# Optimization experiments

Measured on AMD Instinct MI355X. Metric: run time of the kernel, lower is better.

## Reference

```python
import jax, jax.numpy as jnp
import numpy as np
from jax import lax

B, T, D, H, S = 256, 512, 256, 512, 8


def setup_inputs() -> dict:
    key = jax.random.key(0)
    ks = jax.random.split(key, 8)
    bound = 1.0 / np.sqrt(H)  # torch LSTMCell/Linear default init scale
    u = lambda k_, shp: jax.random.uniform(k_, shp, jnp.float32, -bound, bound)
    _input = jax.random.normal(ks[0], (B, T, D), jnp.float32)
    h0 = jax.random.normal(ks[1], (B, H), jnp.float32)
    c0 = jax.random.normal(ks[2], (B, H), jnp.float32)
    W_ih = u(ks[3], (4 * H, D))
    W_hh = u(ks[4], (4 * H, H))
    b_ih = u(ks[5], (4 * H,))
    b_hh = u(ks[6], (4 * H,))
    W_lin = u(ks[7], (D, H))
    b_lin = jnp.zeros((D,), jnp.float32)
    # random skip weights per module logic: w1~Bern; w2=1 if w1==0 else Bern; first S steps (1,0)
    rng = np.random.default_rng(0)
    w1 = rng.integers(0, 2, T)
    w2 = np.where(w1 == 0, 1, rng.integers(0, 2, T))
    w1[:S] = 1
    w2[:S] = 0
    return {
        "_input": _input, "h0": h0, "c0": c0,
        "W_ih": W_ih, "W_hh": W_hh, "b_ih": b_ih, "b_hh": b_hh,
        "W_lin": W_lin, "b_lin": b_lin,
        "w1": jnp.asarray(w1, jnp.int32), "w2": jnp.asarray(w2, jnp.int32),
        "time_steps": T, "skip_size": S,
    }


def _lstm_cell(x, h, c, W_ih, W_hh, b_ih, b_hh):
    gates = x @ W_ih.T + b_ih + h @ W_hh.T + b_hh  # [B, 4H]
    i, f, g, o = jnp.split(gates, 4, axis=-1)
    i, f, o = jax.nn.sigmoid(i), jax.nn.sigmoid(f), jax.nn.sigmoid(o)
    c_new = f * c + i * jnp.tanh(g)
    h_new = o * jnp.tanh(c_new)
    return h_new, c_new


def reference(_input, h0, c0, W_ih, W_hh, b_ih, b_hh, W_lin, b_lin, w1, w2, time_steps, skip_size):
    # decoder-mode RSCN: feed previous linear(h) as next input
    buf_h = jnp.repeat(h0[None], skip_size, axis=0)  # FIFO queue as ring buffer [S,B,H]
    buf_c = jnp.repeat(c0[None], skip_size, axis=0)

    def step(carry, xs):
        h_feed, h, c, bh, bc = carry
        w1t, w2t, t = xs
        h_new, c_new = _lstm_cell(h_feed, h, c, W_ih, W_hh, b_ih, b_hh)
        pos = t % skip_size
        skip_h, skip_c = bh[pos], bc[pos]  # queue.get() (oldest)
        bh = bh.at[pos].set(h_new)          # queue.put(new)
        bc = bc.at[pos].set(c_new)
        a = w1t.astype(h_new.dtype)
        b = w2t.astype(h_new.dtype)
        norm = 1.0 / (a + b)
        comb_h = (a * h_new + b * jnp.tanh(skip_h)) * norm
        comb_c = (a * c_new + b * jnp.tanh(skip_c)) * norm
        out = comb_h @ W_lin.T + b_lin  # [B, D]
        return (out, comb_h, comb_c, bh, bc), out

    xs = (w1[:time_steps], w2[:time_steps], jnp.arange(time_steps))
    carry0 = (_input[:, 0, :], h0, c0, buf_h, buf_c)
    (_, h_fin, c_fin, _, _), outs = lax.scan(step, carry0, xs)
    return outs.transpose(1, 0, 2), h_fin, c_fin  # [B,T,D], final (h, c)
```

## Files before the change

kernel.cpp:

```cpp
#include <hip/hip_runtime.h>
#include <math.h>

#define BB 256
#define TT 512
#define DD 256
#define HH 512
#define SS 8
#define G4H 2048
#define BH (BB*HH)
#define OUT_BASE ((size_t)BB*TT*DD)
#define NGRP 16
#define GR 16
#define XSLOT_U32 4096

typedef _Float16 f16;
typedef __attribute__((ext_vector_type(8)))  _Float16 f16x8;
typedef __attribute__((ext_vector_type(16))) float    f32x16;

__device__ __forceinline__ float sigm(float x) { return 1.f / (1.f + __expf(-x)); }
__device__ __forceinline__ float ftanh(float x) {
  x = fminf(15.f, fmaxf(-15.f, x));
  float e = __expf(-2.f * x);
  return (1.f - e) / (1.f + e);
}


__global__ __launch_bounds__(256) void prep_wbig16(
    const float* __restrict__ W_ih, const float* __restrict__ W_hh,
    const float* __restrict__ W_lin, f16* __restrict__ Wbig16)
{
  __shared__ float As[64][20];
  __shared__ float Bs[16][68];
  const int n0 = blockIdx.x * 64;
  const int j0 = blockIdx.y * 64;
  const int tid = threadIdx.x;
  const int tn = tid >> 4, tj = tid & 15;
  float acc[4][4] = {};
  for (int k0 = 0; k0 < DD; k0 += 16) {
    { int r = tid >> 2, c = (tid & 3) * 4;
      *(float4*)&As[r][c] = *(const float4*)&W_ih[(size_t)(n0 + r) * DD + k0 + c]; }
    { int r = tid >> 4, c = (tid & 15) * 4;
      *(float4*)&Bs[r][c] = *(const float4*)&W_lin[(size_t)(k0 + r) * HH + j0 + c]; }
    __syncthreads();
    #pragma unroll
    for (int k = 0; k < 16; ++k) {
      float a[4], bv[4];
      #pragma unroll
      for (int i = 0; i < 4; ++i) a[i] = As[tn*4+i][k];
      #pragma unroll
      for (int m = 0; m < 4; ++m) bv[m] = Bs[k][tj*4+m];
      #pragma unroll
      for (int i = 0; i < 4; ++i)
        #pragma unroll
        for (int m = 0; m < 4; ++m)
          acc[i][m] = fmaf(a[i], bv[m], acc[i][m]);
    }
    __syncthreads();
  }
  #pragma unroll
  for (int i = 0; i < 4; ++i) {
    int n = n0 + tn*4 + i;
    #pragma unroll
    for (int m = 0; m < 4; ++m) {
      int j = j0 + tj*4 + m;
      Wbig16[(size_t)n*HH + j] = (f16)(acc[i][m] + W_hh[(size_t)n*HH + j]);
    }
  }
}

__global__ void prep_bias(const float* __restrict__ b_ih, const float* __restrict__ b_hh,
                          const float* __restrict__ W_ih, const float* __restrict__ b_lin,
                          float* __restrict__ bias0, float* __restrict__ bias1)
{
  int n = blockIdx.x * 256 + threadIdx.x;
  float s = b_ih[n] + b_hh[n];
  float d = 0.f;
  for (int k = 0; k < DD; ++k) d = fmaf(W_ih[(size_t)n*DD + k], b_lin[k], d);
  bias0[n] = s;
  bias1[n] = s + d;
}

#define NIH (G4H*DD)
#define NHH (G4H*HH)
__global__ void prep_cvtw(const float* __restrict__ W_ih, const float* __restrict__ W_hh,
                          const float* __restrict__ W_lin,
                          f16* __restrict__ Wih16, f16* __restrict__ Whh16,
                          f16* __restrict__ Wlin16)
{
  int e = blockIdx.x * 256 + threadIdx.x;
  if (e < NIH) Wih16[e] = (f16)W_ih[e];
  else if (e < NIH + NHH) Whh16[e - NIH] = (f16)W_hh[e - NIH];
  else Wlin16[e - NIH - NHH] = (f16)W_lin[e - NIH - NHH];
}

__global__ void prep_init(const float* __restrict__ x0, const float* __restrict__ h0,
                          const float* __restrict__ c0,
                          const int* __restrict__ w1, const int* __restrict__ w2,
                          float* __restrict__ bh, float* __restrict__ bc,
                          f16* __restrict__ x0hi, f16* __restrict__ x0lo,
                          f16* __restrict__ h0hi, f16* __restrict__ h0lo,
                          float4* __restrict__ stepc,
                          int* __restrict__ flags)
{
  int e = blockIdx.x * 256 + threadIdx.x;
  int r = e & (BH - 1);
  bh[e] = h0[r];
  bc[e] = c0[r];
  if (e < BH) {
    float v = h0[e];
    f16 hi = (f16)v;
    h0hi[e] = hi;
    h0lo[e] = (f16)(v - (float)hi);
  }
  if (e < BB*DD) {
    int b = e >> 8, d = e & 255;
    float v = x0[(size_t)b*(TT*DD) + d];
    f16 hi = (f16)v;
    x0hi[e] = hi;
    x0lo[e] = (f16)(v - (float)hi);
  }
  if (e < TT) {
    float a1 = (float)w1[e], a2 = (float)w2[e];
    stepc[e] = make_float4(a1, a2, 1.f / (a1 + a2), 0.f);
  }
  if (e < 256) flags[e] = 0;
}


__device__ __forceinline__ void stageG(const unsigned* __restrict__ Xs,
                                       f16* lds, int tid) {
  const int lane = tid & 63;
  const int wv = tid >> 6;
  #pragma unroll
  for (int i = 0; i < 2; ++i) {
    int r = wv * 2 + i;
    const char* src = (const char*)Xs + (size_t)r * 1024 +
                      (size_t)((lane ^ r) & 63) * 16;
    __builtin_amdgcn_global_load_lds(
        (const __attribute__((address_space(1))) void*)src,
        (__attribute__((address_space(3))) void*)((char*)lds + r * 1024),
        16, 0, 0x11 );
  }
}

__device__ __forceinline__ f32x16 gemmS(const f16x8 (&w)[32], const f16* lds, int lane) {
  const int row = lane & 31;
  const int sel = lane >> 5;
  const int rb  = row * 1024;
  const int key = row & 31;
  f32x16 acc;
  #pragma unroll
  for (int i = 0; i < 16; ++i) acc[i] = 0.f;
  #pragma unroll
  for (int ks = 0; ks < 32; ++ks) {
    int gk = 2 * ks + sel;
    int off = rb + (((gk & 31) ^ key) << 4) + ((gk & 32) << 4);
    f16x8 a = *(const f16x8*)((const char*)lds + off);
    acc = __builtin_amdgcn_mfma_f32_32x32x16_f16(a, w[ks], acc, 0, 0, 0);
  }
  return acc;
}

__global__ __launch_bounds__(512, 2) void lstm_persist(
    const f16* __restrict__ x0hi, const f16* __restrict__ x0lo,
    const f16* __restrict__ h0hi, const f16* __restrict__ h0lo,
    const float* __restrict__ c0,
    const f16* __restrict__ Wih16, const f16* __restrict__ Whh16,
    const f16* __restrict__ Wbig16, const f16* __restrict__ Wlin16,
    const float* __restrict__ bias0, const float* __restrict__ bias1,
    const float* __restrict__ b_lin,
    const float4* __restrict__ stepc,
    unsigned* __restrict__ X,
    float* __restrict__ bh, float* __restrict__ bc,
    int* __restrict__ flags,
    float* __restrict__ outp)
{
  __shared__ f16 LdsA[16384];
  __shared__ float gbuf[8192];

  const int tid  = threadIdx.x;
  const int lane = tid & 63;
  const int wv   = tid >> 6;
  const int bid  = blockIdx.x;
  const bool isG = bid < 128;
  const int grp  = isG ? (bid & 15) : (bid - 128);
  const int role = bid >> 4;
  const int b0   = grp * GR;
  const int row  = lane & 31;
  const int ksel8 = (lane >> 5) * 8;

  int* gflag = flags + grp * 16;

  for (int k = tid; k < 8192; k += 512) LdsA[8192 + k] = (f16)0;

  int wrow;
  const f16* wbase;
  if (isG) {
    wrow  = (wv & 3) * 512 + role * 64 + (wv >> 2) * 32 + row;
    wbase = Wbig16 + (size_t)wrow * HH;
  } else {
    wrow  = wv * 32 + row;
    wbase = Wlin16 + (size_t)wrow * HH;
  }
  f16x8 wreg[32];
  #pragma unroll
  for (int ks = 0; ks < 32; ++ks)
    wreg[ks] = *(const f16x8*)(wbase + ks * 16 + ksel8);

  if (isG) {
    int   eidx[2];
    float creg[2];
    const int jl = tid & 63;
    const int jg = role * 64 + jl;
    const float bI = bias1[jg],        bF = bias1[512 + jg];
    const float bG = bias1[1024 + jg], bO = bias1[1536 + jg];
    #pragma unroll
    for (int i = 0; i < 2; ++i) {
      int c = i * 512 + tid;
      int bl = c >> 6;
      eidx[i] = (b0 + bl) * HH + jg;
      creg[i] = c0[eidx[i]];
    }

    for (int t = 0; t < TT; ++t) {
      if (t > 0) {
        if (tid < 8) {
          while (__hip_atomic_load(&gflag[tid], __ATOMIC_RELAXED,
                                   __HIP_MEMORY_SCOPE_AGENT) < t) {}
        } else if (tid == 8 && t >= 4) {
          while (__hip_atomic_load(&gflag[8], __ATOMIC_RELAXED,
                                   __HIP_MEMORY_SCOPE_AGENT) < t - 3) {}
        }
        __syncthreads();
        stageG(X + (size_t)(((t - 1) & 3) * NGRP + grp) * XSLOT_U32, LdsA, tid);
      }

      const float4 sc = stepc[t];
      const int pos = t & (SS - 1);
      float shv[2], scv[2];
      #pragma unroll
      for (int i = 0; i < 2; ++i) {
        int bx = pos * BH + eidx[i];
        shv[i] = bh[bx];
        scv[i] = bc[bx];
      }

      f32x16 acc;
      if (t == 0) {
        #pragma unroll
        for (int i = 0; i < 16; ++i) acc[i] = 0.f;
        const int prow = (b0 + row < BB) ? (b0 + row) : (BB - 1);
        const f16* arh = x0hi + (size_t)prow * DD;
        const f16* arl = x0lo + (size_t)prow * DD;
        const f16* w1p = Wih16 + (size_t)wrow * DD;
        #pragma unroll
        for (int ks = 0; ks < 16; ++ks) {
          int ko = ks * 16 + ksel8;
          f16x8 w = *(const f16x8*)(w1p + ko);
          acc = __builtin_amdgcn_mfma_f32_32x32x16_f16(*(const f16x8*)(arh + ko), w, acc, 0,0,0);
          acc = __builtin_amdgcn_mfma_f32_32x32x16_f16(*(const f16x8*)(arl + ko), w, acc, 0,0,0);
        }
        const f16* brh = h0hi + (size_t)prow * HH;
        const f16* brl = h0lo + (size_t)prow * HH;
        const f16* w2p = Whh16 + (size_t)wrow * HH;
        #pragma unroll
        for (int ks = 0; ks < 32; ++ks) {
          int ko = ks * 16 + ksel8;
          f16x8 w = *(const f16x8*)(w2p + ko);
          acc = __builtin_amdgcn_mfma_f32_32x32x16_f16(*(const f16x8*)(brh + ko), w, acc, 0,0,0);
          acc = __builtin_amdgcn_mfma_f32_32x32x16_f16(*(const f16x8*)(brl + ko), w, acc, 0,0,0);
        }
      } else {
        __syncthreads();
        acc = gemmS(wreg, LdsA, lane);
      }

      {
        const int col = lane & 31;
        const int g4 = wv & 3, jh = wv >> 2;
        #pragma unroll
        for (int rg = 0; rg < 16; ++rg) {
          int m = (rg & 3) + ((rg >> 2) << 3) + ((lane >> 5) << 2);
          if (m < GR)
            gbuf[g4 * 2048 + m * 64 + jh * 32 + col] = acc[rg];
        }
      }
      __syncthreads();

      const float a1 = sc.x, a2 = sc.y, nrm = sc.z;
      float baI = bI, baF = bF, baG = bG, baO = bO;
      if (t == 0) {
        baI = bias0[jg];        baF = bias0[512 + jg];
        baG = bias0[1024 + jg]; baO = bias0[1536 + jg];
      }
      unsigned* Xw = X + (size_t)((t & 3) * NGRP + grp) * XSLOT_U32;
      float hnv[2], cnv[2], chv[2];
      #pragma unroll
      for (int i = 0; i < 2; ++i) {
        int c = i * 512 + tid;
        int bl = c >> 6;
        float pi = gbuf[c]        + baI;
        float pf = gbuf[2048 + c] + baF;
        float pg = gbuf[4096 + c] + baG;
        float po = gbuf[6144 + c] + baO;
        float i_ = sigm(pi), f_ = sigm(pf), o_ = sigm(po), g_ = ftanh(pg);
        float cnew = fmaf(f_, creg[i], i_ * g_);
        float hnew = o_ * ftanh(cnew);
        float ch = (a1 * hnew + a2 * ftanh(shv[i])) * nrm;
        hnv[i] = hnew; cnv[i] = cnew; chv[i] = ch;
        f16 hv = (f16)ch;
        unsigned hb = (unsigned)*(const unsigned short*)&hv;
        unsigned part = (unsigned)__shfl_xor((int)hb, 1);
        if ((tid & 1) == 0)
          __hip_atomic_store(&Xw[bl * 256 + (jg >> 1)], hb | (part << 16),
                             __ATOMIC_RELAXED, __HIP_MEMORY_SCOPE_AGENT);
      }
      __syncthreads();
      if (tid == 0)
        __hip_atomic_store(&gflag[role], t + 1, __ATOMIC_RELAXED,
                           __HIP_MEMORY_SCOPE_AGENT);

      #pragma unroll
      for (int i = 0; i < 2; ++i) {
        float cc = (a1 * cnv[i] + a2 * ftanh(scv[i])) * nrm;
        creg[i] = cc;
        int bx = pos * BH + eidx[i];
        bh[bx] = hnv[i];
        bc[bx] = cnv[i];
        if (t == TT - 1) {
          __builtin_nontemporal_store(chv[i], &outp[OUT_BASE + eidx[i]]);
          __builtin_nontemporal_store(cc,     &outp[OUT_BASE + BH + eidx[i]]);
        }
      }
    }
  } else {
    const float bld = b_lin[wrow];
    for (int s = 0; s < TT; ++s) {
      if (tid < 8) {
        while (__hip_atomic_load(&gflag[tid], __ATOMIC_RELAXED,
                                 __HIP_MEMORY_SCOPE_AGENT) < s + 1) {}
      }
      __syncthreads();
      stageG(X + (size_t)((s & 3) * NGRP + grp) * XSLOT_U32, LdsA, tid);
      __syncthreads();
      f32x16 acc = gemmS(wreg, LdsA, lane);
      __syncthreads();
      if (tid == 0)
        __hip_atomic_store(&gflag[8], s + 1, __ATOMIC_RELAXED,
                           __HIP_MEMORY_SCOPE_AGENT);
      const size_t tbase = (size_t)s * DD + wrow;
      #pragma unroll
      for (int rg = 0; rg < 16; ++rg) {
        int m = (rg & 3) + ((rg >> 2) << 3) + ((lane >> 5) << 2);
        if (m < GR)
          __builtin_nontemporal_store(acc[rg] + bld,
                                      &outp[(size_t)(b0 + m) * (TT*DD) + tbase]);
      }
    }
  }
}


extern "C" void kernel_launch(void* const* d_in, const int* in_sizes, int n_in,
                              void* d_out, int out_size, void* d_ws, size_t ws_size,
                              hipStream_t stream)
{
  const float* x0    = (const float*)d_in[0];
  const float* h0    = (const float*)d_in[1];
  const float* c0    = (const float*)d_in[2];
  const float* W_ih  = (const float*)d_in[3];
  const float* W_hh  = (const float*)d_in[4];
  const float* b_ih  = (const float*)d_in[5];
  const float* b_hh  = (const float*)d_in[6];
  const float* W_lin = (const float*)d_in[7];
  const float* b_lin = (const float*)d_in[8];
  const int*   w1    = (const int*)d_in[9];
  const int*   w2    = (const int*)d_in[10];

  char* p = (char*)d_ws;
  f16* Wbig16 = (f16*)p;            p += (size_t)G4H*HH*2;
  f16* Wih16  = (f16*)p;            p += (size_t)G4H*DD*2;
  f16* Whh16  = (f16*)p;            p += (size_t)G4H*HH*2;
  f16* Wlin16 = (f16*)p;            p += (size_t)DD*HH*2;
  f16* x0hi   = (f16*)p;            p += (size_t)BB*DD*2;
  f16* x0lo   = (f16*)p;            p += (size_t)BB*DD*2;
  f16* h0hi   = (f16*)p;            p += (size_t)BH*2;
  f16* h0lo   = (f16*)p;            p += (size_t)BH*2;
  unsigned* X = (unsigned*)p;       p += (size_t)4*NGRP*XSLOT_U32*4;
  float* bh   = (float*)p;          p += (size_t)SS*BH*4;
  float* bc   = (float*)p;          p += (size_t)SS*BH*4;
  float* bias0= (float*)p;          p += G4H*4;
  float* bias1= (float*)p;          p += G4H*4;
  float4* stepc = (float4*)p;       p += (size_t)TT*16;
  int*  flags = (int*)p;            p += 256*4;
  float* outp = (float*)d_out;

  hipLaunchKernelGGL(prep_wbig16, dim3(32, 8), dim3(256), 0, stream,
                     W_ih, W_hh, W_lin, Wbig16);
  hipLaunchKernelGGL(prep_bias, dim3(8), dim3(256), 0, stream,
                     b_ih, b_hh, W_ih, b_lin, bias0, bias1);
  hipLaunchKernelGGL(prep_cvtw, dim3(6656), dim3(256), 0, stream,
                     W_ih, W_hh, W_lin, Wih16, Whh16, Wlin16);
  hipLaunchKernelGGL(prep_init, dim3(4096), dim3(256), 0, stream,
                     x0, h0, c0, w1, w2, bh, bc, x0hi, x0lo, h0hi, h0lo, stepc, flags);

  hipLaunchKernelGGL(lstm_persist, dim3(128 + NGRP), dim3(512), 0, stream,
                     x0hi, x0lo, h0hi, h0lo, c0, Wih16, Whh16, Wbig16, Wlin16,
                     bias0, bias1, b_lin, stepc, X, bh, bc, flags, outp);
}
```

Measured before the change: 1.741 ms.

## Switch recurrent GEMMs from 32x32 to 16x16x32 MFMA to match 16-row batch groups

Replaces the 32x32x16 MFMA, which wasted half its M rows because each group holds only 16 batch rows, with two 16x16x32 MFMAs per k-step covering the same 32 output columns. This halves LDS staging and the gate buffer, drops the zero-padding of the unused rows, and adds a column rotation in the gate buffer layout to avoid bank conflicts. It is meant to cut MFMA cycles on the serial per-timestep critical path. The cost is new index math for the scatter and gather, which must stay consistent with the swizzled LDS layout.

Result: faster. 1.660 ms (-4.7%).

```diff
diff --git a/kernel.cpp b/kernel.cpp
--- a/kernel.cpp
+++ b/kernel.cpp
@@ -14,8 +14,8 @@
 #define XSLOT_U32 4096
 
 typedef _Float16 f16;
-typedef __attribute__((ext_vector_type(8)))  _Float16 f16x8;
-typedef __attribute__((ext_vector_type(16))) float    f32x16;
+typedef __attribute__((ext_vector_type(8))) _Float16 f16x8;
+typedef __attribute__((ext_vector_type(4))) float    f32x4;
 
 __device__ __forceinline__ float sigm(float x) { return 1.f / (1.f + __expf(-x)); }
 __device__ __forceinline__ float ftanh(float x) {
@@ -143,22 +143,19 @@
   }
 }
 
-__device__ __forceinline__ f32x16 gemmS(const f16x8 (&w)[32], const f16* lds, int lane) {
-  const int row = lane & 31;
-  const int sel = lane >> 5;
-  const int rb  = row * 1024;
-  const int key = row & 31;
-  f32x16 acc;
+__device__ __forceinline__ void gemm16(const f16x8 (&wA)[16], const f16x8 (&wB)[16],
+                                       const f16* lds, int lane,
+                                       f32x4& acc0, f32x4& acc1) {
+  const int r  = lane & 15;
+  const int kc = lane >> 4;
+  const int rb = r * 1024;
   #pragma unroll
-  for (int i = 0; i < 16; ++i) acc[i] = 0.f;
-  #pragma unroll
-  for (int ks = 0; ks < 32; ++ks) {
-    int gk = 2 * ks + sel;
-    int off = rb + (((gk & 31) ^ key) << 4) + ((gk & 32) << 4);
-    f16x8 a = *(const f16x8*)((const char*)lds + off);
-    acc = __builtin_amdgcn_mfma_f32_32x32x16_f16(a, w[ks], acc, 0, 0, 0);
-  }
-  return acc;
+  for (int ks = 0; ks < 16; ++ks) {
+    int u = ks * 4 + kc;
+    f16x8 a = *(const f16x8*)((const char*)lds + rb + ((u ^ r) << 4));
+    acc0 = __builtin_amdgcn_mfma_f32_16x16x32_f16(a, wA[ks], acc0, 0, 0, 0);
+    acc1 = __builtin_amdgcn_mfma_f32_16x16x32_f16(a, wB[ks], acc1, 0, 0, 0);
+  }
 }
 
 __global__ __launch_bounds__(512, 2) void lstm_persist(
@@ -175,8 +172,8 @@
     int* __restrict__ flags,
     float* __restrict__ outp)
 {
-  __shared__ f16 LdsA[16384];
-  __shared__ float gbuf[8192];
+  __shared__ f16 LdsA[8192];
+  __shared__ float gbuf[4096];
 
   const int tid  = threadIdx.x;
   const int lane = tid & 63;
@@ -186,26 +183,29 @@
   const int grp  = isG ? (bid & 15) : (bid - 128);
   const int role = bid >> 4;
   const int b0   = grp * GR;
-  const int row  = lane & 31;
-  const int ksel8 = (lane >> 5) * 8;
+  const int r16  = lane & 15;
+  const int kc   = lane >> 4;
+  const int ksel = kc * 8;
 
   int* gflag = flags + grp * 16;
 
-  for (int k = tid; k < 8192; k += 512) LdsA[8192 + k] = (f16)0;
-
-  int wrow;
-  const f16* wbase;
+  int rowA, rowB;
+  const f16* wsrc;
   if (isG) {
-    wrow  = (wv & 3) * 512 + role * 64 + (wv >> 2) * 32 + row;
-    wbase = Wbig16 + (size_t)wrow * HH;
+    rowA = (wv & 3) * 512 + role * 64 + (wv >> 2) * 32 + r16;
+    rowB = rowA + 16;
+    wsrc = Wbig16;
   } else {
-    wrow  = wv * 32 + row;
-    wbase = Wlin16 + (size_t)wrow * HH;
-  }
-  f16x8 wreg[32];
+    rowA = wv * 32 + r16;
+    rowB = rowA + 16;
+    wsrc = Wlin16;
+  }
+  f16x8 wA[16], wB[16];
   #pragma unroll
-  for (int ks = 0; ks < 32; ++ks)
-    wreg[ks] = *(const f16x8*)(wbase + ks * 16 + ksel8);
+  for (int ks = 0; ks < 16; ++ks) {
+    wA[ks] = *(const f16x8*)(wsrc + (size_t)rowA * HH + ks * 32 + ksel);
+    wB[ks] = *(const f16x8*)(wsrc + (size_t)rowB * HH + ks * 32 + ksel);
+  }
 
   if (isG) {
     int   eidx[2];
@@ -245,44 +245,57 @@
         scv[i] = bc[bx];
       }
 
-      f32x16 acc;
+      f32x4 acc0, acc1;
+      #pragma unroll
+      for (int i = 0; i < 4; ++i) { acc0[i] = 0.f; acc1[i] = 0.f; }
       if (t == 0) {
+        const f16* arh = x0hi + (size_t)(b0 + r16) * DD;
+        const f16* arl = x0lo + (size_t)(b0 + r16) * DD;
+        const f16* wap = Wih16 + (size_t)rowA * DD;
+        const f16* wbp = Wih16 + (size_t)rowB * DD;
         #pragma unroll
-        for (int i = 0; i < 16; ++i) acc[i] = 0.f;
-        const int prow = (b0 + row < BB) ? (b0 + row) : (BB - 1);
-        const f16* arh = x0hi + (size_t)prow * DD;
-        const f16* arl = x0lo + (size_t)prow * DD;
-        const f16* w1p = Wih16 + (size_t)wrow * DD;
+        for (int ks = 0; ks < 8; ++ks) {
+          int ko = ks * 32 + ksel;
+          f16x8 wa = *(const f16x8*)(wap + ko);
+          f16x8 wb = *(const f16x8*)(wbp + ko);
+          f16x8 ah = *(const f16x8*)(arh + ko);
+          f16x8 al = *(const f16x8*)(arl + ko);
+          acc0 = __builtin_amdgcn_mfma_f32_16x16x32_f16(ah, wa, acc0, 0, 0, 0);
+          acc1 = __builtin_amdgcn_mfma_f32_16x16x32_f16(ah, wb, acc1, 0, 0, 0);
+          acc0 = __builtin_amdgcn_mfma_f32_16x16x32_f16(al, wa, acc0, 0, 0, 0);
+          acc1 = __builtin_amdgcn_mfma_f32_16x16x32_f16(al, wb, acc1, 0, 0, 0);
+        }
+        const f16* brh = h0hi + (size_t)(b0 + r16) * HH;
+        const f16* brl = h0lo + (size_t)(b0 + r16) * HH;
+        const f16* qap = Whh16 + (size_t)rowA * HH;
+        const f16* qbp = Whh16 + (size_t)rowB * HH;
         #pragma unroll
         for (int ks = 0; ks < 16; ++ks) {
-          int ko = ks * 16 + ksel8;
-          f16x8 w = *(const f16x8*)(w1p + ko);
-          acc = __builtin_amdgcn_mfma_f32_32x32x16_f16(*(const f16x8*)(arh + ko), w, acc, 0,0,0);
-          acc = __builtin_amdgcn_mfma_f32_32x32x16_f16(*(const f16x8*)(arl + ko), w, acc, 0,0,0);
-        }
-        const f16* brh = h0hi + (size_t)prow * HH;
-        const f16* brl = h0lo + (size_t)prow * HH;
-        const f16* w2p = Whh16 + (size_t)wrow * HH;
-        #pragma unroll
-        for (int ks = 0; ks < 32; ++ks) {
-          int ko = ks * 16 + ksel8;
-          f16x8 w = *(const f16x8*)(w2p + ko);
-          acc = __builtin_amdgcn_mfma_f32_32x32x16_f16(*(const f16x8*)(brh + ko), w, acc, 0,0,0);
-          acc = __builtin_amdgcn_mfma_f32_32x32x16_f16(*(const f16x8*)(brl + ko), w, acc, 0,0,0);
+          int ko = ks * 32 + ksel;
+          f16x8 wa = *(const f16x8*)(qap + ko);
+          f16x8 wb = *(const f16x8*)(qbp + ko);
+          f16x8 ah = *(const f16x8*)(brh + ko);
+          f16x8 al = *(const f16x8*)(brl + ko);
+          acc0 = __builtin_amdgcn_mfma_f32_16x16x32_f16(ah, wa, acc0, 0, 0, 0);
+          acc1 = __builtin_amdgcn_mfma_f32_16x16x32_f16(ah, wb, acc1, 0, 0, 0);
+          acc0 = __builtin_amdgcn_mfma_f32_16x16x32_f16(al, wa, acc0, 0, 0, 0);
+          acc1 = __builtin_amdgcn_mfma_f32_16x16x32_f16(al, wb, acc1, 0, 0, 0);
         }
       } else {
         __syncthreads();
-        acc = gemmS(wreg, LdsA, lane);
+        gemm16(wA, wB, LdsA, lane, acc0, acc1);
       }
 
       {
-        const int col = lane & 31;
         const int g4 = wv & 3, jh = wv >> 2;
         #pragma unroll
-        for (int rg = 0; rg < 16; ++rg) {
-          int m = (rg & 3) + ((rg >> 2) << 3) + ((lane >> 5) << 2);
-          if (m < GR)
-            gbuf[g4 * 2048 + m * 64 + jh * 32 + col] = acc[rg];
+        for (int rg = 0; rg < 4; ++rg) {
+          int m  = kc * 4 + rg;
+          int j0 = jh * 32 + r16;
+          int cs0 = (j0      + 16 * kc) & 63;
+          int cs1 = (j0 + 16 + 16 * kc) & 63;
+          gbuf[g4 * 1024 + m * 64 + cs0] = acc0[rg];
+          gbuf[g4 * 1024 + m * 64 + cs1] = acc1[rg];
         }
       }
       __syncthreads();
@@ -299,10 +312,12 @@
       for (int i = 0; i < 2; ++i) {
         int c = i * 512 + tid;
         int bl = c >> 6;
-        float pi = gbuf[c]        + baI;
-        float pf = gbuf[2048 + c] + baF;
-        float pg = gbuf[4096 + c] + baG;
-        float po = gbuf[6144 + c] + baO;
+        int jj = c & 63;
+        int gofs = bl * 64 + ((jj + 16 * (bl >> 2)) & 63);
+        float pi = gbuf[gofs]        + baI;
+        float pf = gbuf[1024 + gofs] + baF;
+        float pg = gbuf[2048 + gofs] + baG;
+        float po = gbuf[3072 + gofs] + baO;
         float i_ = sigm(pi), f_ = sigm(pf), o_ = sigm(po), g_ = ftanh(pg);
         float cnew = fmaf(f_, creg[i], i_ * g_);
         float hnew = o_ * ftanh(cnew);
@@ -334,7 +349,8 @@
       }
     }
   } else {
-    const float bld = b_lin[wrow];
+    const float bld0 = b_lin[rowA];
+    const float bld1 = b_lin[rowB];
     for (int s = 0; s < TT; ++s) {
       if (tid < 8) {
         while (__hip_atomic_load(&gflag[tid], __ATOMIC_RELAXED,
@@ -343,18 +359,22 @@
       __syncthreads();
       stageG(X + (size_t)((s & 3) * NGRP + grp) * XSLOT_U32, LdsA, tid);
       __syncthreads();
-      f32x16 acc = gemmS(wreg, LdsA, lane);
+      f32x4 acc0, acc1;
+      #pragma unroll
+      for (int i = 0; i < 4; ++i) { acc0[i] = 0.f; acc1[i] = 0.f; }
+      gemm16(wA, wB, LdsA, lane, acc0, acc1);
       __syncthreads();
       if (tid == 0)
         __hip_atomic_store(&gflag[8], s + 1, __ATOMIC_RELAXED,
                            __HIP_MEMORY_SCOPE_AGENT);
-      const size_t tbase = (size_t)s * DD + wrow;
-      #pragma unroll
-      for (int rg = 0; rg < 16; ++rg) {
-        int m = (rg & 3) + ((rg >> 2) << 3) + ((lane >> 5) << 2);
-        if (m < GR)
-          __builtin_nontemporal_store(acc[rg] + bld,
-                                      &outp[(size_t)(b0 + m) * (TT*DD) + tbase]);
+      const size_t tbase = (size_t)s * DD + wv * 32 + r16;
+      #pragma unroll
+      for (int rg = 0; rg < 4; ++rg) {
+        int m = kc * 4 + rg;
+        __builtin_nontemporal_store(acc0[rg] + bld0,
+                                    &outp[(size_t)(b0 + m) * (TT*DD) + tbase]);
+        __builtin_nontemporal_store(acc1[rg] + bld1,
+                                    &outp[(size_t)(b0 + m) * (TT*DD) + tbase + 16]);
       }
     }
   }
```
